# Kernel optimization log

Hardware: AMD Instinct MI355X
Metric: run time of the kernel (lower is better)

Reference implementation:

```python
import jax, jax.numpy as jnp
import numpy as np

N = 40000   # query points
M = 40000   # support points
H = 32      # neighbors per query
CIN = 64
COUT = 64
KS = 3      # kernel points per dim
PDIM = 3
K = KS ** PDIM  # 27 kernel points
RADIUS = 1.0
KP_EXTENT = RADIUS / (KS - 1) * PDIM ** 0.5


def _kernel_points():
    # replicates KPConv.getKernelPoints: grid of KS^PDIM points in a ball of RADIUS
    xyz = np.linspace(-1.0, 1.0, KS)
    pts = np.meshgrid(*PDIM * [xyz])
    pts = np.vstack([p.flatten() for p in pts]).T  # [K, PDIM]
    pts = pts / PDIM ** 0.5
    return (pts * RADIUS).astype(np.float32)


def setup_inputs() -> dict:
    key = jax.random.key(0)
    k1, k2, k3, k4, k5 = jax.random.split(key, 5)
    q_pts = jax.random.uniform(k1, (N, PDIM), dtype=jnp.float32) * 10.0
    s_pts = jax.random.uniform(k2, (M, PDIM), dtype=jnp.float32) * 10.0
    neighb_inds = jax.random.randint(k3, (N, H), 0, M + 1)  # M == shadow index
    x = jax.random.normal(k4, (M, CIN), dtype=jnp.float32)
    # kaiming-uniform-like init for weights [K, CIN, COUT]
    bound = (6.0 / ((1.0 + 5.0) * CIN)) ** 0.5
    weights = jax.random.uniform(k5, (K, CIN, COUT), dtype=jnp.float32,
                                 minval=-bound, maxval=bound)
    kernel_points = jnp.asarray(_kernel_points())
    return {"q_pts": q_pts, "s_pts": s_pts, "neighb_inds": neighb_inds,
            "x": x, "weights": weights, "kernel_points": kernel_points}


def reference(q_pts, s_pts, neighb_inds, x, weights, kernel_points):
    # append shadow support point (far away) and zero shadow feature
    s_pts_p = jnp.concatenate(
        [s_pts, jnp.full((1, s_pts.shape[-1]), 1e6, dtype=s_pts.dtype)], axis=0)
    x_p = jnp.concatenate(
        [x, jnp.zeros((1, x.shape[-1]), dtype=x.dtype)], axis=0)

    neighbors = s_pts_p[neighb_inds] - q_pts[:, None, :]        # [N, H, 3]
    neighb_x = x_p[neighb_inds]                                  # [N, H, CIN]

    # distance of each neighbor to each kernel point
    diff = neighbors[:, :, None, :] - kernel_points              # [N, H, K, 3]
    sq_d = jnp.sum(diff * diff, axis=-1)                         # [N, H, K]
    all_w = jnp.clip(1.0 - jnp.sqrt(sq_d) / KP_EXTENT, 0.0)      # [N, H, K]

    # all_weights^T @ neighb_x  -> [N, K, CIN]
    weighted = jnp.einsum('nhk,nhc->nkc', all_w, neighb_x)
    # per-kernel-point matmul with weights [K, CIN, COUT], summed over K
    out = jnp.einsum('nkc,kco->no', weighted, weights)           # [N, COUT]
    return out
```

## Files before the change

### kernel.cpp

```cpp
#include <hip/hip_runtime.h>

typedef short bf16x8 __attribute__((ext_vector_type(8)));
typedef float f32x4  __attribute__((ext_vector_type(4)));

#define HN    32
#define CIN   64
#define KP    27
#define QB    64
#define CAPB  96
#define NTB   1024
#define OSTR  65

#define QB2   32
#define CAP2  64
#define OSTR2 68

#define INV_EXT 1.1547005383792517f
#define CUT2    3.4821f

__device__ __forceinline__ unsigned f2bf(float f){
    union{float fv;unsigned u;}v; v.fv=f;
    unsigned u=v.u;
    u += 0x7fffu + ((u>>16)&1u);
    return u>>16;
}

__global__ __launch_bounds__(256)
void kp_prep2(const float* __restrict__ s, const float* __restrict__ W,
              float4* __restrict__ o, unsigned short* __restrict__ Wt2, int M)
{
    int tid = blockIdx.x*256 + threadIdx.x;
    if (tid < M) o[tid] = make_float4(s[tid*3+0], s[tid*3+1], s[tid*3+2], 0.f);
    if (tid < KP*8*64){
        int lane = tid & 63;
        int f  = (tid>>6) & 7;
        int kk = tid >> 9;
        int ot = f>>1, ks = f&1, gg = lane>>4;
        unsigned r[8];
#pragma unroll
        for (int j=0;j<8;++j)
            r[j] = f2bf(W[(size_t)kk*4096 + (size_t)(ks*32 + gg*8 + j)*64 + ot*16 + (lane&15)]);
        uint4 v; v.x=r[0]|(r[1]<<16); v.y=r[2]|(r[3]<<16); v.z=r[4]|(r[5]<<16); v.w=r[6]|(r[7]<<16);
        *(uint4*)&Wt2[(size_t)tid*8] = v;
    }
}

__device__ __forceinline__ bf16x8 ldBf(const unsigned short* __restrict__ Wt2, int k, int f, int lane){
    return *(const bf16x8*)(Wt2 + ((size_t)(k*8 + f)*64 + lane)*8);
}
__device__ __forceinline__ void loadB_w(const float* __restrict__ W, int k, int lane, int g,
                                        bf16x8 (&b)[8]){
#pragma unroll
    for (int f=0;f<8;++f){
        int ot=f>>1, ks=f&1;
        union{unsigned u[4]; bf16x8 v;} bb;
#pragma unroll
        for (int jj=0;jj<4;++jj){
            unsigned l0=f2bf(W[(size_t)k*4096 + (size_t)(ks*32+g*8+2*jj)*64   + ot*16+(lane&15)]);
            unsigned l1=f2bf(W[(size_t)k*4096 + (size_t)(ks*32+g*8+2*jj+1)*64 + ot*16+(lane&15)]);
            bb.u[jj]=l0|(l1<<16);
        }
        b[f]=bb.v;
    }
}

__global__ __launch_bounds__(256,4)
void kpconv_fused(const float* __restrict__ q_pts, const int* __restrict__ inds,
                  const float* __restrict__ x, const float* __restrict__ kpts,
                  const float4* __restrict__ sp4, const unsigned short* __restrict__ Wt2,
                  float* __restrict__ out, int N, int M)
{
    __shared__ unsigned short rows[64*CIN];
    __shared__ __align__(16) float wlds[KP*64];
    __shared__ __align__(16) float outacc[QB2*OSTR2];
    __shared__ float qls[QB2*3];
    __shared__ float bx[CAP2], by[CAP2], bz[CAP2];
    __shared__ int bq[CAP2], bixs[CAP2];
    __shared__ int cnt;

    const int t    = threadIdx.x;
    const int lane = t & 63;
    const int wv   = t >> 6;
    const int g    = lane >> 4;
    const int r15  = lane & 15;
    const int nq0  = blockIdx.x * QB2;
    const int NP   = N*HN;

    for (int j=t; j<QB2*OSTR2; j+=256) outacc[j]=0.f;
    for (int j=t; j<QB2*3;    j+=256){ int gi=nq0*3+j; qls[j]=(gi<N*3)? q_pts[gi]:0.f; }
    if (t < CAP2) bq[t]=0;
    if (t==0) cnt=0;
    __syncthreads();

    int idxv[4];
#pragma unroll
    for (int jj=0; jj<4; ++jj){
        int pair = nq0*HN + jj*256 + t;
        idxv[jj] = (pair < NP) ? inds[pair] : M;
    }
    float4 s4v[4];
#pragma unroll
    for (int jj=0; jj<4; ++jj){
        int ic = (idxv[jj] < M) ? idxv[jj] : 0;
        s4v[jj] = sp4[ic];
    }
#pragma unroll
    for (int jj=0; jj<4; ++jj){
        if (idxv[jj] < M){
            int q = (jj*256 + t) >> 5;
            float px=s4v[jj].x-qls[q*3], py=s4v[jj].y-qls[q*3+1], pz=s4v[jj].z-qls[q*3+2];
            if (px*px+py*py+pz*pz <= CUT2){
                int sl = atomicAdd(&cnt, 1);
                if (sl < CAP2){ bx[sl]=px; by[sl]=py; bz[sl]=pz; bq[sl]=q; bixs[sl]=idxv[jj]; }
            }
        }
    }
    __syncthreads();
    const int total = cnt;

    auto process = [&](int cc){
        const int nrow = (cc + 15) & ~15;
        int itA=t, itB=t+256;
        int rlA=itA>>3, c8A=itA&7, rlB=itB>>3, c8B=itB&7;
        bool vA=(rlA<cc), vB=(rlB<cc);
        bool wrA=(rlA<nrow), wrB=(rlB<nrow);
        int ixA = vA ? bixs[rlA] : bixs[0];
        int ixB = vB ? bixs[rlB] : bixs[0];
        const float4* xrA = (const float4*)(x + (size_t)ixA*CIN);
        const float4* xrB = (const float4*)(x + (size_t)ixB*CIN);
        float4 fA0=xrA[c8A*2], fA1=xrA[c8A*2+1];
        float4 fB0=xrB[c8B*2], fB1=xrB[c8B*2+1];
        for (int i=t; i<KP*64; i+=256){
            int row = i&63;
            if (row >= nrow) continue;
            int k = i>>6;
            float w=0.f;
            if (row < cc){
                float dx=bx[row]-kpts[k*3+0];
                float dy=by[row]-kpts[k*3+1];
                float dz=bz[row]-kpts[k*3+2];
                w = fmaxf(1.f - sqrtf(dx*dx+dy*dy+dz*dz)*INV_EXT, 0.f);
            }
            wlds[i]=w;
        }
        if (wrA){
            uint4 v; v.x=0u; v.y=0u; v.z=0u; v.w=0u;
            if (vA){
                v.x=f2bf(fA0.x)|(f2bf(fA0.y)<<16); v.y=f2bf(fA0.z)|(f2bf(fA0.w)<<16);
                v.z=f2bf(fA1.x)|(f2bf(fA1.y)<<16); v.w=f2bf(fA1.z)|(f2bf(fA1.w)<<16);
            }
            *(uint4*)((char*)rows + rlA*128 + ((c8A*16)^((rlA&7)<<4))) = v;
        }
        if (wrB){
            uint4 v; v.x=0u; v.y=0u; v.z=0u; v.w=0u;
            if (vB){
                v.x=f2bf(fB0.x)|(f2bf(fB0.y)<<16); v.y=f2bf(fB0.z)|(f2bf(fB0.w)<<16);
                v.z=f2bf(fB1.x)|(f2bf(fB1.y)<<16); v.w=f2bf(fB1.z)|(f2bf(fB1.w)<<16);
            }
            *(uint4*)((char*)rows + rlB*128 + ((c8B*16)^((rlB&7)<<4))) = v;
        }
        __syncthreads();

        const char* rb = (const char*)rows;
        bool rtv[4];
        bf16x8 A0[4], A1[4];
#pragma unroll
        for (int rt=0; rt<4; ++rt){
            rtv[rt] = (rt*16) < cc;
            int row = rt*16 + r15;
            int rc  = rtv[rt] ? row : r15;
            A0[rt] = *(const bf16x8*)(rb + rc*128 + (( g*16)   ^((rc&7)<<4)));
            A1[rt] = *(const bf16x8*)(rb + rc*128 + ((64+g*16) ^((rc&7)<<4)));
        }
        f32x4 acc[4];
#pragma unroll
        for (int rt=0; rt<4; ++rt){ f32x4 z={0.f,0.f,0.f,0.f}; acc[rt]=z; }

        const int f0 = wv*2, f1 = wv*2+1;
        bf16x8 Ba0 = ldBf(Wt2, 0, f0, lane);
        bf16x8 Ba1 = ldBf(Wt2, 0, f1, lane);
        bf16x8 Bb0 = ldBf(Wt2, 1, f0, lane);
        bf16x8 Bb1 = ldBf(Wt2, 1, f1, lane);
#pragma unroll 1
        for (int k=0; k<KP; ++k){
            int kf = (k+2 < KP) ? (k+2) : k;
            bf16x8 Bf0 = ldBf(Wt2, kf, f0, lane);
            bf16x8 Bf1 = ldBf(Wt2, kf, f1, lane);
            const float* wk = &wlds[k*64];
#pragma unroll
            for (int rt=0; rt<4; ++rt){
                if (!rtv[rt]) continue;
                f32x4 w4 = *(const f32x4*)(wk + rt*16 + g*4);
                bool act = __any(w4[0]>0.f || w4[1]>0.f || w4[2]>0.f || w4[3]>0.f);
                if (act){
                    f32x4 c={0.f,0.f,0.f,0.f};
                    c = __builtin_amdgcn_mfma_f32_16x16x32_bf16(A0[rt], Ba0, c, 0,0,0);
                    c = __builtin_amdgcn_mfma_f32_16x16x32_bf16(A1[rt], Ba1, c, 0,0,0);
                    acc[rt][0] += w4[0]*c[0];
                    acc[rt][1] += w4[1]*c[1];
                    acc[rt][2] += w4[2]*c[2];
                    acc[rt][3] += w4[3]*c[3];
                }
            }
            Ba0 = Bb0; Ba1 = Bb1;
            Bb0 = Bf0; Bb1 = Bf1;
        }
#pragma unroll
        for (int rt=0; rt<4; ++rt){
            if (!rtv[rt]) continue;
            int rbase = rt*16 + g*4;
#pragma unroll
            for (int rr=0; rr<4; ++rr){
                float val = acc[rt][rr];
                int qv = bq[rbase+rr];
                if (val != 0.f)
                    atomicAdd(&outacc[qv*OSTR2 + wv*16 + r15], val);
            }
        }
        __syncthreads();
    };

    if (total <= CAP2){
        if (total > 0) process(total);
    } else {
        for (int w=0; w<(QB2*HN)/64; ++w){
            __syncthreads();
            if (t==0) cnt=0;
            __syncthreads();
            if (t < 64){
                int pl = w*64 + t, pair = nq0*HN + pl;
                if (pair < NP){
                    int idx = inds[pair];
                    if ((unsigned)idx < (unsigned)M){
                        int q = pl >> 5;
                        float4 s4 = sp4[idx];
                        float px=s4.x-qls[q*3], py=s4.y-qls[q*3+1], pz=s4.z-qls[q*3+2];
                        if (px*px+py*py+pz*pz <= CUT2){
                            int sl = atomicAdd(&cnt, 1);
                            bx[sl]=px; by[sl]=py; bz[sl]=pz; bq[sl]=q; bixs[sl]=idx;
                        }
                    }
                }
            }
            __syncthreads();
            if (cnt > 0) process(cnt);
        }
    }
    __syncthreads();

    for (int j=t; j<QB2*16; j+=256){
        int q=j>>4, o4=j&15, n=nq0+q;
        if (n < N)
            ((float4*)out)[(size_t)n*16 + o4] = *(const float4*)&outacc[q*OSTR2 + o4*4];
    }
}


__global__ __launch_bounds__(NTB)
void kpconv6(const float* __restrict__ q_pts, const float* __restrict__ s_pts,
             const int* __restrict__ inds, const float* __restrict__ x,
             const float* __restrict__ W, const float* __restrict__ kpts,
             float* __restrict__ out, int N, int M)
{
    __shared__ float qls[QB*3];
    __shared__ float posx[CAPB], posy[CAPB], posz[CAPB];
    __shared__ int   eqb[CAPB], eidxb[CAPB];
    __shared__ unsigned short rows[CAPB*CIN];
    __shared__ float outacc[QB*OSTR];
    __shared__ int   cnt;

    const int t    = threadIdx.x;
    const int lane = t & 63;
    const int wv   = t >> 6;
    const int g    = lane >> 4;
    const int r15  = lane & 15;
    const int nq0  = blockIdx.x * QB;

    const int k0 = wv, k1 = wv + 16;
    const bool has2 = (k1 < KP);

    bf16x8 B0[8], B1[8];
    loadB_w(W, k0, lane, g, B0);
    loadB_w(W, has2 ? k1 : k0, lane, g, B1);
    const float k0x=kpts[k0*3+0], k0y=kpts[k0*3+1], k0z=kpts[k0*3+2];
    float k1x=0.f,k1y=0.f,k1z=0.f;
    if (has2){ k1x=kpts[k1*3+0]; k1y=kpts[k1*3+1]; k1z=kpts[k1*3+2]; }

    for (int j=t; j<QB*OSTR; j+=NTB) outacc[j]=0.f;
    for (int j=t; j<QB*3;   j+=NTB){ int gi=nq0*3+j; qls[j]=(gi<N*3)? q_pts[gi]:0.f; }
    if (t==0) cnt=0;
    __syncthreads();

    auto process = [&](int cc){
        if (cc<=0) return;
        const int ntile=(cc+15)>>4, nrow=ntile*16;
        for (int j=cc+t; j<nrow; j+=NTB){ posx[j]=1e9f; posy[j]=1e9f; posz[j]=1e9f; eqb[j]=0; }
        for (int it=t; it<nrow*8; it+=NTB){
            int e=it>>3, c8=it&7;
            uint4 v; v.x=0u; v.y=0u; v.z=0u; v.w=0u;
            if (e<cc){
                const float4* xr=(const float4*)(x+(size_t)eidxb[e]*CIN);
                float4 f0=xr[c8*2], f1=xr[c8*2+1];
                v.x=f2bf(f0.x)|(f2bf(f0.y)<<16); v.y=f2bf(f0.z)|(f2bf(f0.w)<<16);
                v.z=f2bf(f1.x)|(f2bf(f1.y)<<16); v.w=f2bf(f1.z)|(f2bf(f1.w)<<16);
            }
            int ba=e*128+((c8*16)^((e&7)<<4));
            *(uint4*)((char*)rows+ba)=v;
        }
        __syncthreads();
        for (int tile=0; tile<ntile; ++tile){
            const char* rb=(const char*)rows;
            int row=tile*16+r15;
            bf16x8 a0=*(const bf16x8*)(rb+row*128+((g*16)    ^((row&7)<<4)));
            bf16x8 a1=*(const bf16x8*)(rb+row*128+((64+g*16) ^((row&7)<<4)));
            int rbase=tile*16+g*4;
            float w0[4], w1[4]; int qq[4];
#pragma unroll
            for (int r=0;r<4;++r){
                float sx=posx[rbase+r], sy=posy[rbase+r], sz=posz[rbase+r];
                qq[r]=eqb[rbase+r];
                float dx=sx-k0x, dy=sy-k0y, dz=sz-k0z;
                w0[r]=fmaxf(1.f-sqrtf(dx*dx+dy*dy+dz*dz)*INV_EXT,0.f);
                float ex=sx-k1x, ey=sy-k1y, ez=sz-k1z;
                float w1r=fmaxf(1.f-sqrtf(ex*ex+ey*ey+ez*ez)*INV_EXT,0.f);
                w1[r]=has2? w1r : 0.f;
            }
#pragma unroll
            for (int ot=0;ot<4;++ot){
                f32x4 c={0.f,0.f,0.f,0.f};
                c=__builtin_amdgcn_mfma_f32_16x16x32_bf16(a0,B0[2*ot],c,0,0,0);
                c=__builtin_amdgcn_mfma_f32_16x16x32_bf16(a1,B0[2*ot+1],c,0,0,0);
                f32x4 d={0.f,0.f,0.f,0.f};
                if (has2){
                    d=__builtin_amdgcn_mfma_f32_16x16x32_bf16(a0,B1[2*ot],d,0,0,0);
                    d=__builtin_amdgcn_mfma_f32_16x16x32_bf16(a1,B1[2*ot+1],d,0,0,0);
                }
#pragma unroll
                for (int r=0;r<4;++r){
                    float val=w0[r]*c[r]+w1[r]*d[r];
                    if (val!=0.f) atomicAdd(&outacc[qq[r]*OSTR+ot*16+r15], val);
                }
            }
        }
        __syncthreads();
    };

    for (int it=t; it<QB*HN; it+=NTB){
        int q=it>>5, h=it&31, n=nq0+q;
        bool inr=false; int idx=0; float px=0.f,py=0.f,pz=0.f;
        if (n<N){
            idx=inds[(size_t)n*HN+h];
            if ((unsigned)idx<(unsigned)M){
                float sx=s_pts[idx*3], sy=s_pts[idx*3+1], sz=s_pts[idx*3+2];
                px=sx-qls[q*3]; py=sy-qls[q*3+1]; pz=sz-qls[q*3+2];
                inr=(px*px+py*py+pz*pz)<=CUT2;
            }
        }
        if (inr){
            int sl=atomicAdd(&cnt,1);
            if (sl<CAPB){ eqb[sl]=q; eidxb[sl]=idx; posx[sl]=px; posy[sl]=py; posz[sl]=pz; }
        }
    }
    __syncthreads();
    const int total=cnt;

    if (total<=CAPB){
        process(total);
    } else {
        for (int w=0; w<(QB*HN)/64; ++w){
            __syncthreads();
            if (t==0) cnt=0;
            __syncthreads();
            if (t<64){
                int pair=w*64+t;
                int q=pair>>5, h=pair&31, n=nq0+q;
                if (n<N){
                    int idx=inds[(size_t)n*HN+h];
                    if ((unsigned)idx<(unsigned)M){
                        float sx=s_pts[idx*3], sy=s_pts[idx*3+1], sz=s_pts[idx*3+2];
                        float px=sx-qls[q*3], py=sy-qls[q*3+1], pz=sz-qls[q*3+2];
                        if (px*px+py*py+pz*pz<=CUT2){
                            int sl=atomicAdd(&cnt,1);
                            eqb[sl]=q; eidxb[sl]=idx; posx[sl]=px; posy[sl]=py; posz[sl]=pz;
                        }
                    }
                }
            }
            __syncthreads();
            process(cnt);
        }
    }
    __syncthreads();

    for (int j=t; j<QB*CIN; j+=NTB){
        int q=j>>6, o=j&63, n=nq0+q;
        if (n<N) out[(size_t)n*CIN+o]=outacc[q*OSTR+o];
    }
}

extern "C" void kernel_launch(void* const* d_in, const int* in_sizes, int n_in,
                              void* d_out, int out_size, void* d_ws, size_t ws_size,
                              hipStream_t stream)
{
    const float* q_pts=(const float*)d_in[0];
    const float* s_pts=(const float*)d_in[1];
    const int*   inds =(const int*)d_in[2];
    const float* x    =(const float*)d_in[3];
    const float* W    =(const float*)d_in[4];
    const float* kpts =(const float*)d_in[5];
    float* outp=(float*)d_out;
    int N=in_sizes[0]/3;
    int M=in_sizes[1]/3;

    char* wsb=(char*)d_ws;
    float4* sp4=(float4*)wsb;
    unsigned short* Wt2=(unsigned short*)(wsb + (size_t)M*16);

    const size_t WT2B = (size_t)KP*8*64*8*2;
    size_t need = (size_t)M*16 + WT2B;

    if (ws_size >= need){
        int prepN = (M > KP*8*64) ? M : KP*8*64;
        hipLaunchKernelGGL(kp_prep2, dim3((prepN+255)/256), dim3(256), 0, stream,
                           s_pts, W, sp4, Wt2, M);
        int nblocks = (N + QB2 - 1) / QB2;
        hipLaunchKernelGGL(kpconv_fused, dim3(nblocks), dim3(256), 0, stream,
                           q_pts, inds, x, kpts, sp4, Wt2, outp, N, M);
        return;
    }

    hipLaunchKernelGGL(kpconv6, dim3((N+QB-1)/QB), dim3(NTB), 0, stream,
                       q_pts, s_pts, inds, x, W, kpts, outp, N, M);
}
```

Measured before the change: 46.73 us.

## Halve queries per block to shrink LDS and registers, raising occupancy

```diff
diff --git a/kernel.cpp b/kernel.cpp
--- a/kernel.cpp
+++ b/kernel.cpp
@@ -11,8 +11,9 @@
 #define NTB   1024
 #define OSTR  65
 
-#define QB2   32
-#define CAP2  64
+#define QB2   16
+#define CAP2  48
+#define WL    48
 #define OSTR2 68
 
 #define INV_EXT 1.1547005383792517f
@@ -64,14 +65,14 @@
     }
 }
 
-__global__ __launch_bounds__(256,4)
+__global__ __launch_bounds__(256,6)
 void kpconv_fused(const float* __restrict__ q_pts, const int* __restrict__ inds,
                   const float* __restrict__ x, const float* __restrict__ kpts,
                   const float4* __restrict__ sp4, const unsigned short* __restrict__ Wt2,
                   float* __restrict__ out, int N, int M)
 {
-    __shared__ unsigned short rows[64*CIN];
-    __shared__ __align__(16) float wlds[KP*64];
+    __shared__ unsigned short rows[CAP2*CIN];
+    __shared__ __align__(16) float wlds[KP*WL];
     __shared__ __align__(16) float outacc[QB2*OSTR2];
     __shared__ float qls[QB2*3];
     __shared__ float bx[CAP2], by[CAP2], bz[CAP2];
@@ -87,25 +88,25 @@
     const int NP   = N*HN;
 
     for (int j=t; j<QB2*OSTR2; j+=256) outacc[j]=0.f;
-    for (int j=t; j<QB2*3;    j+=256){ int gi=nq0*3+j; qls[j]=(gi<N*3)? q_pts[gi]:0.f; }
+    if (t < QB2*3){ int gi=nq0*3+t; qls[t]=(gi<N*3)? q_pts[gi]:0.f; }
     if (t < CAP2) bq[t]=0;
     if (t==0) cnt=0;
     __syncthreads();
 
-    int idxv[4];
-#pragma unroll
-    for (int jj=0; jj<4; ++jj){
+    int idxv[2];
+#pragma unroll
+    for (int jj=0; jj<2; ++jj){
         int pair = nq0*HN + jj*256 + t;
         idxv[jj] = (pair < NP) ? inds[pair] : M;
     }
-    float4 s4v[4];
-#pragma unroll
-    for (int jj=0; jj<4; ++jj){
+    float4 s4v[2];
+#pragma unroll
+    for (int jj=0; jj<2; ++jj){
         int ic = (idxv[jj] < M) ? idxv[jj] : 0;
         s4v[jj] = sp4[ic];
     }
 #pragma unroll
-    for (int jj=0; jj<4; ++jj){
+    for (int jj=0; jj<2; ++jj){
         if (idxv[jj] < M){
             int q = (jj*256 + t) >> 5;
             float px=s4v[jj].x-qls[q*3], py=s4v[jj].y-qls[q*3+1], pz=s4v[jj].z-qls[q*3+2];
@@ -130,18 +131,16 @@
         const float4* xrB = (const float4*)(x + (size_t)ixB*CIN);
         float4 fA0=xrA[c8A*2], fA1=xrA[c8A*2+1];
         float4 fB0=xrB[c8B*2], fB1=xrB[c8B*2+1];
-        for (int i=t; i<KP*64; i+=256){
-            int row = i&63;
-            if (row >= nrow) continue;
-            int k = i>>6;
-            float w=0.f;
-            if (row < cc){
-                float dx=bx[row]-kpts[k*3+0];
-                float dy=by[row]-kpts[k*3+1];
-                float dz=bz[row]-kpts[k*3+2];
-                w = fmaxf(1.f - sqrtf(dx*dx+dy*dy+dz*dz)*INV_EXT, 0.f);
-            }
-            wlds[i]=w;
+        for (int k = wv; k < KP; k += 4){
+            float kx=kpts[k*3+0], ky=kpts[k*3+1], kz=kpts[k*3+2];
+            if (lane < nrow){
+                float w=0.f;
+                if (lane < cc){
+                    float dx=bx[lane]-kx, dy=by[lane]-ky, dz=bz[lane]-kz;
+                    w = fmaxf(1.f - sqrtf(dx*dx+dy*dy+dz*dz)*INV_EXT, 0.f);
+                }
+                wlds[k*WL + lane]=w;
+            }
         }
         if (wrA){
             uint4 v; v.x=0u; v.y=0u; v.z=0u; v.w=0u;
@@ -162,51 +161,48 @@
         __syncthreads();
 
         const char* rb = (const char*)rows;
-        bool rtv[4];
-        bf16x8 A0[4], A1[4];
-#pragma unroll
-        for (int rt=0; rt<4; ++rt){
+        bool rtv[3];
+        bf16x8 A0[3], A1[3];
+#pragma unroll
+        for (int rt=0; rt<3; ++rt){
             rtv[rt] = (rt*16) < cc;
             int row = rt*16 + r15;
             int rc  = rtv[rt] ? row : r15;
             A0[rt] = *(const bf16x8*)(rb + rc*128 + (( g*16)   ^((rc&7)<<4)));
             A1[rt] = *(const bf16x8*)(rb + rc*128 + ((64+g*16) ^((rc&7)<<4)));
         }
-        f32x4 acc[4];
-#pragma unroll
-        for (int rt=0; rt<4; ++rt){ f32x4 z={0.f,0.f,0.f,0.f}; acc[rt]=z; }
+        f32x4 acc[3];
+#pragma unroll
+        for (int rt=0; rt<3; ++rt){ f32x4 z={0.f,0.f,0.f,0.f}; acc[rt]=z; }
 
         const int f0 = wv*2, f1 = wv*2+1;
-        bf16x8 Ba0 = ldBf(Wt2, 0, f0, lane);
-        bf16x8 Ba1 = ldBf(Wt2, 0, f1, lane);
-        bf16x8 Bb0 = ldBf(Wt2, 1, f0, lane);
-        bf16x8 Bb1 = ldBf(Wt2, 1, f1, lane);
+        bf16x8 Bc0 = ldBf(Wt2, 0, f0, lane);
+        bf16x8 Bc1 = ldBf(Wt2, 0, f1, lane);
 #pragma unroll 1
         for (int k=0; k<KP; ++k){
-            int kf = (k+2 < KP) ? (k+2) : k;
-            bf16x8 Bf0 = ldBf(Wt2, kf, f0, lane);
-            bf16x8 Bf1 = ldBf(Wt2, kf, f1, lane);
-            const float* wk = &wlds[k*64];
-#pragma unroll
-            for (int rt=0; rt<4; ++rt){
+            int kn = (k+1 < KP) ? (k+1) : k;
+            bf16x8 Bn0 = ldBf(Wt2, kn, f0, lane);
+            bf16x8 Bn1 = ldBf(Wt2, kn, f1, lane);
+            const float* wk = &wlds[k*WL];
+#pragma unroll
+            for (int rt=0; rt<3; ++rt){
                 if (!rtv[rt]) continue;
                 f32x4 w4 = *(const f32x4*)(wk + rt*16 + g*4);
                 bool act = __any(w4[0]>0.f || w4[1]>0.f || w4[2]>0.f || w4[3]>0.f);
                 if (act){
                     f32x4 c={0.f,0.f,0.f,0.f};
-                    c = __builtin_amdgcn_mfma_f32_16x16x32_bf16(A0[rt], Ba0, c, 0,0,0);
-                    c = __builtin_amdgcn_mfma_f32_16x16x32_bf16(A1[rt], Ba1, c, 0,0,0);
+                    c = __builtin_amdgcn_mfma_f32_16x16x32_bf16(A0[rt], Bc0, c, 0,0,0);
+                    c = __builtin_amdgcn_mfma_f32_16x16x32_bf16(A1[rt], Bc1, c, 0,0,0);
                     acc[rt][0] += w4[0]*c[0];
                     acc[rt][1] += w4[1]*c[1];
                     acc[rt][2] += w4[2]*c[2];
                     acc[rt][3] += w4[3]*c[3];
                 }
             }
-            Ba0 = Bb0; Ba1 = Bb1;
-            Bb0 = Bf0; Bb1 = Bf1;
-        }
-#pragma unroll
-        for (int rt=0; rt<4; ++rt){
+            Bc0 = Bn0; Bc1 = Bn1;
+        }
+#pragma unroll
+        for (int rt=0; rt<3; ++rt){
             if (!rtv[rt]) continue;
             int rbase = rt*16 + g*4;
 #pragma unroll
@@ -223,12 +219,12 @@
     if (total <= CAP2){
         if (total > 0) process(total);
     } else {
-        for (int w=0; w<(QB2*HN)/64; ++w){
+        for (int w=0; w<(QB2*HN)/32; ++w){
             __syncthreads();
             if (t==0) cnt=0;
             __syncthreads();
-            if (t < 64){
-                int pl = w*64 + t, pair = nq0*HN + pl;
+            if (t < 32){
+                int pl = w*32 + t, pair = nq0*HN + pl;
                 if (pair < NP){
                     int idx = inds[pair];
                     if ((unsigned)idx < (unsigned)M){
@@ -248,8 +244,8 @@
     }
     __syncthreads();
 
-    for (int j=t; j<QB2*16; j+=256){
-        int q=j>>4, o4=j&15, n=nq0+q;
+    if (t < QB2*16){
+        int q=t>>4, o4=t&15, n=nq0+q;
         if (n < N)
             ((float4*)out)[(size_t)n*16 + o4] = *(const float4*)&outacc[q*OSTR2 + o4*4];
     }
```

New measurement: 48.61 us. 1.04x slower.
